# Performance work log

Hardware: AMD Instinct MI355X
Metric: run time of the kernel (lower is better)

The kernel has to match this reference:

```python
import jax, jax.numpy as jnp
import numpy as np


def setup_inputs() -> dict:
    key = jax.random.key(0)
    ks = jax.random.split(key, 6)
    B, T, E, H, K = 4, 2048, 1024, 16, 3
    x = jax.random.normal(ks[0], (B, T, E), dtype=jnp.float32)
    mem_k = jax.random.normal(ks[1], (B, T, K, E), dtype=jnp.float32)
    mem_v = jax.random.normal(ks[2], (B, T, K, E), dtype=jnp.float32)
    W_attn = jax.random.normal(ks[3], (E, 3 * E), dtype=jnp.float32) * 0.02
    W_proj = jax.random.normal(ks[4], (E, E), dtype=jnp.float32) * 0.02
    gate_bias = jax.random.normal(ks[5], (H, 1, 1), dtype=jnp.float32)
    return {"x": x, "mem_k": mem_k, "mem_v": mem_v, "W_attn": W_attn,
            "W_proj": W_proj, "gate_bias": gate_bias}


def reference(x, mem_k, mem_v, W_attn, W_proj, gate_bias):
    B, T, E = x.shape
    H = gate_bias.shape[0]
    D = E // H
    K = mem_k.shape[2]
    # qkv projection (no bias)
    qkv = x @ W_attn                                   # [B,T,3E]
    q, k, v = jnp.split(qkv, 3, axis=-1)
    q = q.reshape(B, T, H, D).transpose(0, 2, 1, 3)    # [B,H,T,D]
    k = k.reshape(B, T, H, D).transpose(0, 2, 1, 3)
    v = v.reshape(B, T, H, D).transpose(0, 2, 1, 3)
    # causal SDPA (torch default scale = 1/sqrt(head_dim))
    scores = jnp.einsum('bhqd,bhkd->bhqk', q, k) / jnp.sqrt(jnp.asarray(D, q.dtype))
    causal = jnp.tril(jnp.ones((T, T), dtype=bool))
    scores = jnp.where(causal, scores, jnp.finfo(scores.dtype).min)
    attn = jax.nn.softmax(scores, axis=-1)
    y = jnp.einsum('bhqk,bhkd->bhqd', attn, v)         # [B,H,T,D]
    # top-k retrieved memory attention (k small, here 3)
    mk = mem_k.reshape(B, T, K, H, D).transpose(0, 3, 1, 2, 4)  # [B,H,T,K,D]
    mv = mem_v.reshape(B, T, K, H, D).transpose(0, 3, 1, 2, 4)
    # faithful to source: scale = n_embd / n_head**(-0.5) = E*sqrt(H)
    mem_scale = jnp.asarray(E, q.dtype) * jnp.sqrt(jnp.asarray(H, q.dtype))
    mem_qk = jnp.einsum('bhtd,bhtkd->bhtk', q, mk) * mem_scale
    mem_qk = jax.nn.softmax(mem_qk, axis=-1)
    mem_qkv = jnp.einsum('bhtk,bhtkd->bhtd', mem_qk, mv)  # [B,H,T,D]
    # gated fusion, gate_bias broadcasts [H,1,1] over [B,H,T,D]
    combined = mem_qkv * gate_bias + y * (1.0 - gate_bias)
    combined = combined.transpose(0, 2, 1, 3).reshape(B, T, E)
    out = combined @ W_proj
    return out
```

## Files before the change

### kernel.cpp

```cpp
#include <hip/hip_runtime.h>
#include <math.h>

#define Bsz 4
#define Tseq 2048
#define Ed 1024
#define Hh 16
#define E3 (3*Ed)
#define MROWS (Bsz*Tseq)

typedef short short8 __attribute__((ext_vector_type(8)));
typedef _Float16 half8 __attribute__((ext_vector_type(8)));
typedef float floatx4 __attribute__((ext_vector_type(4)));

__device__ __forceinline__ unsigned short f2bf(float f) {
  unsigned int u = __builtin_bit_cast(unsigned int, f);
  u += 0x7fffu + ((u >> 16) & 1u);
  return (unsigned short)(u >> 16);
}
__device__ __forceinline__ float bf2f(unsigned short u) {
  return __builtin_bit_cast(float, ((unsigned int)u) << 16);
}
__device__ __forceinline__ unsigned short f2h(float f) {
  _Float16 h = (_Float16)f;
  return __builtin_bit_cast(unsigned short, h);
}
__device__ __forceinline__ float h2f(unsigned short u) {
  return (float)__builtin_bit_cast(_Float16, u);
}
__device__ __forceinline__ int swz(int row, int col) {
  return row * 64 + ((((col >> 3) ^ (row & 7)) << 3) | (col & 7));
}

__global__ __launch_bounds__(256)
void cast_split_k(const float* __restrict__ s, unsigned short* __restrict__ bb,
                  unsigned short* __restrict__ hh, unsigned short* __restrict__ ll,
                  int n4) {
  int i = blockIdx.x * 256 + threadIdx.x;
  if (i >= n4) return;
  float4 v = ((const float4*)s)[i];
  float vv[4] = {v.x, v.y, v.z, v.w};
  unsigned short ob[4], oh[4], ol[4];
  #pragma unroll
  for (int j = 0; j < 4; ++j) {
    ob[j] = f2bf(vv[j]);
    unsigned short h = f2h(vv[j]);
    oh[j] = h;
    ol[j] = f2h(vv[j] - h2f(h));
  }
  ((uint2*)bb)[i] = *(uint2*)ob;
  ((uint2*)hh)[i] = *(uint2*)oh;
  ((uint2*)ll)[i] = *(uint2*)ol;
}

__global__ __launch_bounds__(256)
void transpose_cast(const float* __restrict__ src, int ld, int c0,
                    unsigned short* __restrict__ dst, int Krows) {
  __shared__ float t[64][65];
  const int kb = blockIdx.y * 64, nb = blockIdx.x * 64;
  const int tid = threadIdx.x;
  #pragma unroll
  for (int i = 0; i < 4; ++i) {
    int u = tid + i * 256;
    int r = u >> 4, c4 = u & 15;
    float4 v = *(const float4*)(src + (size_t)(kb + r) * ld + c0 + nb + c4 * 4);
    t[r][c4*4+0] = v.x; t[r][c4*4+1] = v.y; t[r][c4*4+2] = v.z; t[r][c4*4+3] = v.w;
  }
  __syncthreads();
  #pragma unroll
  for (int i = 0; i < 2; ++i) {
    int u = tid + i * 256;
    int rn = u >> 3, g = u & 7;
    unsigned short o[8];
    #pragma unroll
    for (int j = 0; j < 8; ++j) o[j] = f2bf(t[g*8+j][rn]);
    *(uint4*)(dst + (size_t)(nb + rn) * Krows + kb + g * 8) = *(uint4*)o;
  }
}

__global__ __launch_bounds__(256)
void transpose_split(const float* __restrict__ src, int ld, int c0,
                     unsigned short* __restrict__ dh, unsigned short* __restrict__ dl,
                     int Krows) {
  __shared__ float t[64][65];
  const int kb = blockIdx.y * 64, nb = blockIdx.x * 64;
  const int tid = threadIdx.x;
  #pragma unroll
  for (int i = 0; i < 4; ++i) {
    int u = tid + i * 256;
    int r = u >> 4, c4 = u & 15;
    float4 v = *(const float4*)(src + (size_t)(kb + r) * ld + c0 + nb + c4 * 4);
    t[r][c4*4+0] = v.x; t[r][c4*4+1] = v.y; t[r][c4*4+2] = v.z; t[r][c4*4+3] = v.w;
  }
  __syncthreads();
  #pragma unroll
  for (int i = 0; i < 2; ++i) {
    int u = tid + i * 256;
    int rn = u >> 3, g = u & 7;
    unsigned short oh[8], ol[8];
    #pragma unroll
    for (int j = 0; j < 8; ++j) {
      float f = t[g*8+j][rn];
      unsigned short h = f2h(f);
      oh[j] = h;
      ol[j] = f2h(f - h2f(h));
    }
    size_t off = (size_t)(nb + rn) * Krows + kb + g * 8;
    *(uint4*)(dh + off) = *(uint4*)oh;
    *(uint4*)(dl + off) = *(uint4*)ol;
  }
}

template<int N, int KD, bool OBF>
__global__ __launch_bounds__(256)
void gemm_bf16(const unsigned short* __restrict__ A,
               const unsigned short* __restrict__ Bt,
               void* __restrict__ C) {
  __shared__ __align__(16) unsigned short As[128][72];
  __shared__ __align__(16) unsigned short Bs[128][72];
  const int tid = threadIdx.x;
  const int w = tid >> 6, L = tid & 63, Ln = L & 15, Lq = L >> 4;
  const int wm = w & 1, wn = w >> 1;
  const int m0 = blockIdx.y * 128, n0 = blockIdx.x * 128;

  floatx4 acc[4][4];
  #pragma unroll
  for (int mt = 0; mt < 4; ++mt)
    #pragma unroll
    for (int nt = 0; nt < 4; ++nt) acc[mt][nt] = (floatx4)0.f;

  for (int kt = 0; kt < KD; kt += 64) {
    #pragma unroll
    for (int i = 0; i < 4; ++i) {
      int u = tid + i * 256;
      int row = u >> 3, g = u & 7;
      *(uint4*)&As[row][g*8] = *(const uint4*)(A + (size_t)(m0 + row) * KD + kt + g * 8);
      *(uint4*)&Bs[row][g*8] = *(const uint4*)(Bt + (size_t)(n0 + row) * KD + kt + g * 8);
    }
    __syncthreads();
    #pragma unroll
    for (int kc = 0; kc < 2; ++kc) {
      short8 af[4], bfr[4];
      #pragma unroll
      for (int mt = 0; mt < 4; ++mt)
        af[mt] = *(const short8*)&As[wm*64 + mt*16 + Ln][kc*32 + Lq*8];
      #pragma unroll
      for (int nt = 0; nt < 4; ++nt)
        bfr[nt] = *(const short8*)&Bs[wn*64 + nt*16 + Ln][kc*32 + Lq*8];
      #pragma unroll
      for (int mt = 0; mt < 4; ++mt)
        #pragma unroll
        for (int nt = 0; nt < 4; ++nt)
          acc[mt][nt] = __builtin_amdgcn_mfma_f32_16x16x32_bf16(af[mt], bfr[nt], acc[mt][nt], 0, 0, 0);
    }
    __syncthreads();
  }
  #pragma unroll
  for (int mt = 0; mt < 4; ++mt)
    #pragma unroll
    for (int nt = 0; nt < 4; ++nt)
      #pragma unroll
      for (int r = 0; r < 4; ++r) {
        size_t row = m0 + wm*64 + mt*16 + Lq*4 + r;
        int col = n0 + wn*64 + nt*16 + Ln;
        if (OBF) ((unsigned short*)C)[row * N + col] = f2bf(acc[mt][nt][r]);
        else     ((float*)C)[row * N + col] = acc[mt][nt][r];
      }
}

template<int N, int KD>
__global__ __launch_bounds__(256)
void gemm_f16x3(const unsigned short* __restrict__ Ah,
                const unsigned short* __restrict__ Al,
                const unsigned short* __restrict__ Bh,
                const unsigned short* __restrict__ Bl,
                float* __restrict__ C) {
  __shared__ __align__(16) unsigned short As[2][128][40];
  __shared__ __align__(16) unsigned short Bs[2][128][40];
  const int tid = threadIdx.x;
  const int w = tid >> 6, L = tid & 63, Ln = L & 15, Lq = L >> 4;
  const int wm = w & 1, wn = w >> 1;
  const int m0 = blockIdx.y * 128, n0 = blockIdx.x * 128;

  floatx4 acc[4][4];
  #pragma unroll
  for (int mt = 0; mt < 4; ++mt)
    #pragma unroll
    for (int nt = 0; nt < 4; ++nt) acc[mt][nt] = (floatx4)0.f;

  for (int kt = 0; kt < KD; kt += 32) {
    #pragma unroll
    for (int i = 0; i < 2; ++i) {
      int u = tid + i * 256;
      int row = u >> 2, g = u & 3;
      size_t offA = (size_t)(m0 + row) * KD + kt + g * 8;
      size_t offB = (size_t)(n0 + row) * KD + kt + g * 8;
      *(uint4*)&As[0][row][g*8] = *(const uint4*)(Ah + offA);
      *(uint4*)&As[1][row][g*8] = *(const uint4*)(Al + offA);
      *(uint4*)&Bs[0][row][g*8] = *(const uint4*)(Bh + offB);
      *(uint4*)&Bs[1][row][g*8] = *(const uint4*)(Bl + offB);
    }
    __syncthreads();
    half8 afh[4], afl[4], bfh[4], bfl[4];
    #pragma unroll
    for (int mt = 0; mt < 4; ++mt) {
      afh[mt] = *(const half8*)&As[0][wm*64 + mt*16 + Ln][Lq*8];
      afl[mt] = *(const half8*)&As[1][wm*64 + mt*16 + Ln][Lq*8];
    }
    #pragma unroll
    for (int nt = 0; nt < 4; ++nt) {
      bfh[nt] = *(const half8*)&Bs[0][wn*64 + nt*16 + Ln][Lq*8];
      bfl[nt] = *(const half8*)&Bs[1][wn*64 + nt*16 + Ln][Lq*8];
    }
    #pragma unroll
    for (int mt = 0; mt < 4; ++mt)
      #pragma unroll
      for (int nt = 0; nt < 4; ++nt) {
        acc[mt][nt] = __builtin_amdgcn_mfma_f32_16x16x32_f16(afh[mt], bfh[nt], acc[mt][nt], 0, 0, 0);
        acc[mt][nt] = __builtin_amdgcn_mfma_f32_16x16x32_f16(afh[mt], bfl[nt], acc[mt][nt], 0, 0, 0);
        acc[mt][nt] = __builtin_amdgcn_mfma_f32_16x16x32_f16(afl[mt], bfh[nt], acc[mt][nt], 0, 0, 0);
      }
    __syncthreads();
  }
  #pragma unroll
  for (int mt = 0; mt < 4; ++mt)
    #pragma unroll
    for (int nt = 0; nt < 4; ++nt)
      #pragma unroll
      for (int r = 0; r < 4; ++r) {
        size_t row = m0 + wm*64 + mt*16 + Lq*4 + r;
        int col = n0 + wn*64 + nt*16 + Ln;
        C[row * N + col] = acc[mt][nt][r];
      }
}

__global__ __launch_bounds__(256)
void flash_mfma(const float* __restrict__ qf, const unsigned short* __restrict__ kv,
                unsigned short* __restrict__ y) {
  __shared__ __align__(16) unsigned short Ks[2][64 * 64];
  __shared__ __align__(16) unsigned short Vt[2][64 * 64];
  __shared__ __align__(16) unsigned short Ps[4][32 * 64];
  const int ib = blockIdx.x;
  const int bh = blockIdx.y;
  const int b = bh >> 4, h = bh & 15;
  const int tid = threadIdx.x;
  const int w = tid >> 6, L = tid & 63;
  const int Ln = L & 15, Lq = L >> 4;
  const size_t base = (size_t)b * Tseq;
  const int hof = h * 64;

  for (int t = 0; t < 2; ++t) {
    const int qt = t ? ib : 15 - ib;
    const int q0 = qt * 128;
    const int nkt = 2 * qt + 2;

    short8 qfr[2][2];
    #pragma unroll
    for (int mt = 0; mt < 2; ++mt) {
      const float* qp = qf + (base + q0 + w*32 + mt*16 + Ln) * Ed + hof;
      #pragma unroll
      for (int kc = 0; kc < 2; ++kc) {
        float v[8];
        *(float4*)&v[0] = *(const float4*)(qp + kc*32 + Lq*8);
        *(float4*)&v[4] = *(const float4*)(qp + kc*32 + Lq*8 + 4);
        short8 tt;
        #pragma unroll
        for (int j = 0; j < 8; ++j) tt[j] = (short)f2bf(v[j]);
        qfr[mt][kc] = tt;
      }
    }

    float m_i[2][4], l_i[2][4];
    floatx4 O[2][4];
    #pragma unroll
    for (int mt = 0; mt < 2; ++mt) {
      #pragma unroll
      for (int r = 0; r < 4; ++r) { m_i[mt][r] = -3.0e38f; l_i[mt][r] = 0.f; }
      #pragma unroll
      for (int nt = 0; nt < 4; ++nt) O[mt][nt] = (floatx4)0.f;
    }

    #pragma unroll
    for (int i = 0; i < 2; ++i) {
      int u = tid + i * 256;
      int c = u >> 3, g = u & 7;
      const unsigned short* kvp = kv + (base + c) * 2048 + hof + g * 8;
      uint4 k4 = *(const uint4*)kvp;
      *(uint4*)&Ks[0][c*64 + ((g ^ (c & 7)) << 3)] = k4;
      unsigned short vv[8];
      *(uint4*)vv = *(const uint4*)(kvp + 1024);
      #pragma unroll
      for (int j = 0; j < 8; ++j) Vt[0][swz(g*8 + j, c)] = vv[j];
    }
    __syncthreads();

    int cur = 0;
    for (int kt = 0; kt < nkt; ++kt) {
      uint4 kreg[2], vreg[2];
      const bool pre = (kt + 1 < nkt);
      if (pre) {
        #pragma unroll
        for (int i = 0; i < 2; ++i) {
          int u = tid + i * 256;
          int c = u >> 3, g = u & 7;
          const unsigned short* kvp = kv + (base + (kt+1)*64 + c) * 2048 + hof + g * 8;
          kreg[i] = *(const uint4*)kvp;
          vreg[i] = *(const uint4*)(kvp + 1024);
        }
      }

      short8 kb[4][2];
      #pragma unroll
      for (int nt = 0; nt < 4; ++nt) {
        int krow = nt*16 + Ln;
        #pragma unroll
        for (int kc = 0; kc < 2; ++kc)
          kb[nt][kc] = *(const short8*)&Ks[cur][krow*64 + ((((kc*4 + Lq) ^ (krow & 7)) << 3))];
      }
      floatx4 S[2][4];
      #pragma unroll
      for (int mt = 0; mt < 2; ++mt)
        #pragma unroll
        for (int nt = 0; nt < 4; ++nt) {
          floatx4 a = (floatx4)0.f;
          a = __builtin_amdgcn_mfma_f32_16x16x32_bf16(qfr[mt][0], kb[nt][0], a, 0, 0, 0);
          a = __builtin_amdgcn_mfma_f32_16x16x32_bf16(qfr[mt][1], kb[nt][1], a, 0, 0, 0);
          S[mt][nt] = a;
        }
      #pragma unroll
      for (int mt = 0; mt < 2; ++mt)
        #pragma unroll
        for (int nt = 0; nt < 4; ++nt)
          #pragma unroll
          for (int r = 0; r < 4; ++r) S[mt][nt][r] *= 0.125f;
      if (kt >= 2*qt) {
        #pragma unroll
        for (int mt = 0; mt < 2; ++mt) {
          int rowg = q0 + w*32 + mt*16 + Lq*4;
          #pragma unroll
          for (int nt = 0; nt < 4; ++nt) {
            int colg = kt*64 + nt*16 + Ln;
            #pragma unroll
            for (int r = 0; r < 4; ++r)
              if (colg > rowg + r) S[mt][nt][r] = -3.0e38f;
          }
        }
      }

      #pragma unroll
      for (int mt = 0; mt < 2; ++mt) {
        #pragma unroll
        for (int r = 0; r < 4; ++r) {
          float mx = fmaxf(fmaxf(S[mt][0][r], S[mt][1][r]),
                           fmaxf(S[mt][2][r], S[mt][3][r]));
          mx = fmaxf(mx, __shfl_xor(mx, 1));
          mx = fmaxf(mx, __shfl_xor(mx, 2));
          mx = fmaxf(mx, __shfl_xor(mx, 4));
          mx = fmaxf(mx, __shfl_xor(mx, 8));
          float mnew = fmaxf(m_i[mt][r], mx);
          float alpha = __expf(m_i[mt][r] - mnew);
          m_i[mt][r] = mnew;
          float rs = 0.f;
          #pragma unroll
          for (int nt = 0; nt < 4; ++nt) {
            float p = __expf(S[mt][nt][r] - mnew);
            S[mt][nt][r] = p;
            rs += p;
          }
          rs += __shfl_xor(rs, 1);
          rs += __shfl_xor(rs, 2);
          rs += __shfl_xor(rs, 4);
          rs += __shfl_xor(rs, 8);
          l_i[mt][r] = l_i[mt][r] * alpha + rs;
          #pragma unroll
          for (int nt = 0; nt < 4; ++nt) O[mt][nt][r] *= alpha;
          int prow = mt*16 + Lq*4 + r;
          #pragma unroll
          for (int nt = 0; nt < 4; ++nt)
            Ps[w][swz(prow, nt*16 + Ln)] = f2bf(S[mt][nt][r]);
        }
      }

      short8 vb[4][2], pf[2][2];
      #pragma unroll
      for (int nt = 0; nt < 4; ++nt) {
        int vrow = nt*16 + Ln;
        #pragma unroll
        for (int kc = 0; kc < 2; ++kc)
          vb[nt][kc] = *(const short8*)&Vt[cur][vrow*64 + ((((kc*4 + Lq) ^ (vrow & 7)) << 3))];
      }
      #pragma unroll
      for (int mt = 0; mt < 2; ++mt) {
        int prow = mt*16 + Ln;
        #pragma unroll
        for (int kc = 0; kc < 2; ++kc)
          pf[mt][kc] = *(const short8*)&Ps[w][prow*64 + ((((kc*4 + Lq) ^ (prow & 7)) << 3))];
      }
      #pragma unroll
      for (int mt = 0; mt < 2; ++mt)
        #pragma unroll
        for (int nt = 0; nt < 4; ++nt) {
          O[mt][nt] = __builtin_amdgcn_mfma_f32_16x16x32_bf16(pf[mt][0], vb[nt][0], O[mt][nt], 0, 0, 0);
          O[mt][nt] = __builtin_amdgcn_mfma_f32_16x16x32_bf16(pf[mt][1], vb[nt][1], O[mt][nt], 0, 0, 0);
        }

      if (pre) {
        #pragma unroll
        for (int i = 0; i < 2; ++i) {
          int u = tid + i * 256;
          int c = u >> 3, g = u & 7;
          *(uint4*)&Ks[cur^1][c*64 + ((g ^ (c & 7)) << 3)] = kreg[i];
          unsigned short vv[8];
          *(uint4*)vv = vreg[i];
          #pragma unroll
          for (int j = 0; j < 8; ++j) Vt[cur^1][swz(g*8 + j, c)] = vv[j];
        }
      }
      __syncthreads();
      cur ^= 1;
    }

    #pragma unroll
    for (int mt = 0; mt < 2; ++mt) {
      #pragma unroll
      for (int r = 0; r < 4; ++r) {
        float inv = 1.f / l_i[mt][r];
        size_t rb = (base + q0 + w*32 + mt*16 + Lq*4 + r) * Ed + hof;
        #pragma unroll
        for (int nt = 0; nt < 4; ++nt)
          y[rb + nt*16 + Ln] = f2bf(O[mt][nt][r] * inv);
      }
    }
  }
}

__global__ __launch_bounds__(256)
void mem_gate(const float* __restrict__ qf, const float* __restrict__ mem_k,
              const float* __restrict__ mem_v, const float* __restrict__ gate,
              unsigned short* __restrict__ y) {
  const int tid = threadIdx.x;
  const int lane = tid & 63;
  const int g = (blockIdx.x << 2) | (tid >> 6);
  const int h = g & 15;
  const int bt = g >> 4;
  const float q = qf[(size_t)bt * Ed + h*64 + lane];
  const size_t mb = ((size_t)bt * 3) * Ed + h*64 + lane;

  float s[3];
  #pragma unroll
  for (int k = 0; k < 3; ++k) {
    float p = q * mem_k[mb + (size_t)k * Ed];
    p += __shfl_xor(p, 1);  p += __shfl_xor(p, 2);  p += __shfl_xor(p, 4);
    p += __shfl_xor(p, 8);  p += __shfl_xor(p, 16); p += __shfl_xor(p, 32);
    s[k] = p * 4096.0f;
  }
  float mx = fmaxf(s[0], fmaxf(s[1], s[2]));
  float w0 = __expf(s[0] - mx), w1 = __expf(s[1] - mx), w2 = __expf(s[2] - mx);
  float inv = 1.f / (w0 + w1 + w2);
  float ov = (w0 * mem_v[mb] + w1 * mem_v[mb + Ed] + w2 * mem_v[mb + 2*Ed]) * inv;
  float gb = gate[h];
  unsigned short* yp = y + (size_t)bt * Ed + h*64 + lane;
  float yv = bf2f(*yp);
  *yp = f2bf(ov * gb + yv * (1.f - gb));
}

extern "C" void kernel_launch(void* const* d_in, const int* in_sizes, int n_in,
                              void* d_out, int out_size, void* d_ws, size_t ws_size,
                              hipStream_t stream) {
  const float* x      = (const float*)d_in[0];
  const float* mem_k  = (const float*)d_in[1];
  const float* mem_v  = (const float*)d_in[2];
  const float* W_attn = (const float*)d_in[3];
  const float* W_proj = (const float*)d_in[4];
  const float* gate   = (const float*)d_in[5];
  float* out = (float*)d_out;

  float* qf32          = (float*)d_ws;
  unsigned short* kvb  = (unsigned short*)(qf32 + (size_t)MROWS*Ed);
  unsigned short* ybf  = kvb + (size_t)MROWS*2048;
  unsigned short* xb   = ybf + (size_t)MROWS*Ed;
  unsigned short* wkv  = xb  + (size_t)MROWS*Ed;
  unsigned short* wp   = wkv + (size_t)2048*Ed;
  unsigned short* xh  = (unsigned short*)d_out;
  unsigned short* xl  = xh + (size_t)MROWS*Ed;
  unsigned short* wqh = kvb;
  unsigned short* wql = wqh + (size_t)Ed*Ed;

  cast_split_k<<<(MROWS*Ed/4 + 255)/256, 256, 0, stream>>>(x, xb, xh, xl, MROWS*Ed/4);
  transpose_split<<<dim3(Ed/64, Ed/64), 256, 0, stream>>>(W_attn, E3, 0, wqh, wql, Ed);
  transpose_cast<<<dim3(2048/64, Ed/64), 256, 0, stream>>>(W_attn, E3, Ed, wkv, Ed);
  transpose_cast<<<dim3(Ed/64, Ed/64), 256, 0, stream>>>(W_proj, Ed, 0, wp, Ed);
  gemm_f16x3<Ed, Ed>
      <<<dim3(Ed/128, MROWS/128), 256, 0, stream>>>(xh, xl, wqh, wql, qf32);
  gemm_bf16<2048, Ed, true>
      <<<dim3(2048/128, MROWS/128), 256, 0, stream>>>(xb, wkv, kvb);
  flash_mfma<<<dim3(8, Bsz*Hh), 256, 0, stream>>>(qf32, kvb, ybf);
  mem_gate<<<(MROWS*Hh)/4, 256, 0, stream>>>(qf32, mem_k, mem_v, gate, ybf);
  gemm_bf16<Ed, Ed, false>
      <<<dim3(Ed/128, MROWS/128), 256, 0, stream>>>(ybf, wp, out);
}
```

Measured before the change: 608.5 us.

## Split flash attention query tile across eight waves of sixteen rows

The flash attention kernel now launches 512 threads per block, and each of eight waves owns 16 query rows instead of four waves owning 32 rows. Per-wave register state (O, S, m, l) halves and the K/V tile load is spread over twice as many threads. The intent is more latency hiding through higher wave count per CU. The cost is that every wave reloads the same K/V fragments from LDS for half the MFMA work, so LDS traffic per FLOP roughly doubles.

Measured after the change: 528.4 us. -13.2%, faster.

```diff
diff --git a/kernel.cpp b/kernel.cpp
--- a/kernel.cpp
+++ b/kernel.cpp
@@ -233,12 +233,12 @@
       }
 }
 
-__global__ __launch_bounds__(256)
+__global__ __launch_bounds__(512, 4)
 void flash_mfma(const float* __restrict__ qf, const unsigned short* __restrict__ kv,
                 unsigned short* __restrict__ y) {
   __shared__ __align__(16) unsigned short Ks[2][64 * 64];
   __shared__ __align__(16) unsigned short Vt[2][64 * 64];
-  __shared__ __align__(16) unsigned short Ps[4][32 * 64];
+  __shared__ __align__(16) unsigned short Ps[8][16 * 64];
   const int ib = blockIdx.x;
   const int bh = blockIdx.y;
   const int b = bh >> 4, h = bh & 15;
@@ -253,10 +253,9 @@
     const int q0 = qt * 128;
     const int nkt = 2 * qt + 2;
 
-    short8 qfr[2][2];
-    #pragma unroll
-    for (int mt = 0; mt < 2; ++mt) {
-      const float* qp = qf + (base + q0 + w*32 + mt*16 + Ln) * Ed + hof;
+    short8 qfr[2];
+    {
+      const float* qp = qf + (base + q0 + w*16 + Ln) * Ed + hof;
       #pragma unroll
       for (int kc = 0; kc < 2; ++kc) {
         float v[8];
@@ -265,24 +264,19 @@
         short8 tt;
         #pragma unroll
         for (int j = 0; j < 8; ++j) tt[j] = (short)f2bf(v[j]);
-        qfr[mt][kc] = tt;
-      }
-    }
-
-    float m_i[2][4], l_i[2][4];
-    floatx4 O[2][4];
-    #pragma unroll
-    for (int mt = 0; mt < 2; ++mt) {
-      #pragma unroll
-      for (int r = 0; r < 4; ++r) { m_i[mt][r] = -3.0e38f; l_i[mt][r] = 0.f; }
-      #pragma unroll
-      for (int nt = 0; nt < 4; ++nt) O[mt][nt] = (floatx4)0.f;
-    }
-
-    #pragma unroll
-    for (int i = 0; i < 2; ++i) {
-      int u = tid + i * 256;
-      int c = u >> 3, g = u & 7;
+        qfr[kc] = tt;
+      }
+    }
+
+    float m_i[4], l_i[4];
+    floatx4 O[4];
+    #pragma unroll
+    for (int r = 0; r < 4; ++r) { m_i[r] = -3.0e38f; l_i[r] = 0.f; }
+    #pragma unroll
+    for (int nt = 0; nt < 4; ++nt) O[nt] = (floatx4)0.f;
+
+    {
+      int c = tid >> 3, g = tid & 7;
       const unsigned short* kvp = kv + (base + c) * 2048 + hof + g * 8;
       uint4 k4 = *(const uint4*)kvp;
       *(uint4*)&Ks[0][c*64 + ((g ^ (c & 7)) << 3)] = k4;
@@ -295,17 +289,13 @@
 
     int cur = 0;
     for (int kt = 0; kt < nkt; ++kt) {
-      uint4 kreg[2], vreg[2];
+      uint4 kreg, vreg;
       const bool pre = (kt + 1 < nkt);
+      const int c = tid >> 3, g = tid & 7;
       if (pre) {
-        #pragma unroll
-        for (int i = 0; i < 2; ++i) {
-          int u = tid + i * 256;
-          int c = u >> 3, g = u & 7;
-          const unsigned short* kvp = kv + (base + (kt+1)*64 + c) * 2048 + hof + g * 8;
-          kreg[i] = *(const uint4*)kvp;
-          vreg[i] = *(const uint4*)(kvp + 1024);
-        }
+        const unsigned short* kvp = kv + (base + (kt+1)*64 + c) * 2048 + hof + g * 8;
+        kreg = *(const uint4*)kvp;
+        vreg = *(const uint4*)(kvp + 1024);
       }
 
       short8 kb[4][2];
@@ -316,71 +306,60 @@
         for (int kc = 0; kc < 2; ++kc)
           kb[nt][kc] = *(const short8*)&Ks[cur][krow*64 + ((((kc*4 + Lq) ^ (krow & 7)) << 3))];
       }
-      floatx4 S[2][4];
-      #pragma unroll
-      for (int mt = 0; mt < 2; ++mt)
+      floatx4 S[4];
+      #pragma unroll
+      for (int nt = 0; nt < 4; ++nt) {
+        floatx4 a = (floatx4)0.f;
+        a = __builtin_amdgcn_mfma_f32_16x16x32_bf16(qfr[0], kb[nt][0], a, 0, 0, 0);
+        a = __builtin_amdgcn_mfma_f32_16x16x32_bf16(qfr[1], kb[nt][1], a, 0, 0, 0);
+        S[nt] = a;
+      }
+      #pragma unroll
+      for (int nt = 0; nt < 4; ++nt)
+        #pragma unroll
+        for (int r = 0; r < 4; ++r) S[nt][r] *= 0.125f;
+      if (kt >= 2*qt) {
+        int rowg = q0 + w*16 + Lq*4;
         #pragma unroll
         for (int nt = 0; nt < 4; ++nt) {
-          floatx4 a = (floatx4)0.f;
-          a = __builtin_amdgcn_mfma_f32_16x16x32_bf16(qfr[mt][0], kb[nt][0], a, 0, 0, 0);
-          a = __builtin_amdgcn_mfma_f32_16x16x32_bf16(qfr[mt][1], kb[nt][1], a, 0, 0, 0);
-          S[mt][nt] = a;
+          int colg = kt*64 + nt*16 + Ln;
+          #pragma unroll
+          for (int r = 0; r < 4; ++r)
+            if (colg > rowg + r) S[nt][r] = -3.0e38f;
         }
-      #pragma unroll
-      for (int mt = 0; mt < 2; ++mt)
+      }
+
+      #pragma unroll
+      for (int r = 0; r < 4; ++r) {
+        float mx = fmaxf(fmaxf(S[0][r], S[1][r]), fmaxf(S[2][r], S[3][r]));
+        mx = fmaxf(mx, __shfl_xor(mx, 1));
+        mx = fmaxf(mx, __shfl_xor(mx, 2));
+        mx = fmaxf(mx, __shfl_xor(mx, 4));
+        mx = fmaxf(mx, __shfl_xor(mx, 8));
+        float mnew = fmaxf(m_i[r], mx);
+        float alpha = __expf(m_i[r] - mnew);
+        m_i[r] = mnew;
+        float rs = 0.f;
+        #pragma unroll
+        for (int nt = 0; nt < 4; ++nt) {
+          float p = __expf(S[nt][r] - mnew);
+          S[nt][r] = p;
+          rs += p;
+        }
+        rs += __shfl_xor(rs, 1);
+        rs += __shfl_xor(rs, 2);
+        rs += __shfl_xor(rs, 4);
+        rs += __shfl_xor(rs, 8);
+        l_i[r] = l_i[r] * alpha + rs;
+        #pragma unroll
+        for (int nt = 0; nt < 4; ++nt) O[nt][r] *= alpha;
+        int prow = Lq*4 + r;
         #pragma unroll
         for (int nt = 0; nt < 4; ++nt)
-          #pragma unroll
-          for (int r = 0; r < 4; ++r) S[mt][nt][r] *= 0.125f;
-      if (kt >= 2*qt) {
-        #pragma unroll
-        for (int mt = 0; mt < 2; ++mt) {
-          int rowg = q0 + w*32 + mt*16 + Lq*4;
-          #pragma unroll
-          for (int nt = 0; nt < 4; ++nt) {
-            int colg = kt*64 + nt*16 + Ln;
-            #pragma unroll
-            for (int r = 0; r < 4; ++r)
-              if (colg > rowg + r) S[mt][nt][r] = -3.0e38f;
-          }
-        }
-      }
-
-      #pragma unroll
-      for (int mt = 0; mt < 2; ++mt) {
-        #pragma unroll
-        for (int r = 0; r < 4; ++r) {
-          float mx = fmaxf(fmaxf(S[mt][0][r], S[mt][1][r]),
-                           fmaxf(S[mt][2][r], S[mt][3][r]));
-          mx = fmaxf(mx, __shfl_xor(mx, 1));
-          mx = fmaxf(mx, __shfl_xor(mx, 2));
-          mx = fmaxf(mx, __shfl_xor(mx, 4));
-          mx = fmaxf(mx, __shfl_xor(mx, 8));
-          float mnew = fmaxf(m_i[mt][r], mx);
-          float alpha = __expf(m_i[mt][r] - mnew);
-          m_i[mt][r] = mnew;
-          float rs = 0.f;
-          #pragma unroll
-          for (int nt = 0; nt < 4; ++nt) {
-            float p = __expf(S[mt][nt][r] - mnew);
-            S[mt][nt][r] = p;
-            rs += p;
-          }
-          rs += __shfl_xor(rs, 1);
-          rs += __shfl_xor(rs, 2);
-          rs += __shfl_xor(rs, 4);
-          rs += __shfl_xor(rs, 8);
-          l_i[mt][r] = l_i[mt][r] * alpha + rs;
-          #pragma unroll
-          for (int nt = 0; nt < 4; ++nt) O[mt][nt][r] *= alpha;
-          int prow = mt*16 + Lq*4 + r;
-          #pragma unroll
-          for (int nt = 0; nt < 4; ++nt)
-            Ps[w][swz(prow, nt*16 + Ln)] = f2bf(S[mt][nt][r]);
-        }
-      }
-
-      short8 vb[4][2], pf[2][2];
+          Ps[w][swz(prow, nt*16 + Ln)] = f2bf(S[nt][r]);
+      }
+
+      short8 vb[4][2], pf[2];
       #pragma unroll
       for (int nt = 0; nt < 4; ++nt) {
         int vrow = nt*16 + Ln;
@@ -388,47 +367,36 @@
         for (int kc = 0; kc < 2; ++kc)
           vb[nt][kc] = *(const short8*)&Vt[cur][vrow*64 + ((((kc*4 + Lq) ^ (vrow & 7)) << 3))];
       }
-      #pragma unroll
-      for (int mt = 0; mt < 2; ++mt) {
-        int prow = mt*16 + Ln;
+      {
+        int prow = Ln;
         #pragma unroll
         for (int kc = 0; kc < 2; ++kc)
-          pf[mt][kc] = *(const short8*)&Ps[w][prow*64 + ((((kc*4 + Lq) ^ (prow & 7)) << 3))];
-      }
-      #pragma unroll
-      for (int mt = 0; mt < 2; ++mt)
-        #pragma unroll
-        for (int nt = 0; nt < 4; ++nt) {
-          O[mt][nt] = __builtin_amdgcn_mfma_f32_16x16x32_bf16(pf[mt][0], vb[nt][0], O[mt][nt], 0, 0, 0);
-          O[mt][nt] = __builtin_amdgcn_mfma_f32_16x16x32_bf16(pf[mt][1], vb[nt][1], O[mt][nt], 0, 0, 0);
-        }
+          pf[kc] = *(const short8*)&Ps[w][prow*64 + ((((kc*4 + Lq) ^ (prow & 7)) << 3))];
+      }
+      #pragma unroll
+      for (int nt = 0; nt < 4; ++nt) {
+        O[nt] = __builtin_amdgcn_mfma_f32_16x16x32_bf16(pf[0], vb[nt][0], O[nt], 0, 0, 0);
+        O[nt] = __builtin_amdgcn_mfma_f32_16x16x32_bf16(pf[1], vb[nt][1], O[nt], 0, 0, 0);
+      }
 
       if (pre) {
-        #pragma unroll
-        for (int i = 0; i < 2; ++i) {
-          int u = tid + i * 256;
-          int c = u >> 3, g = u & 7;
-          *(uint4*)&Ks[cur^1][c*64 + ((g ^ (c & 7)) << 3)] = kreg[i];
-          unsigned short vv[8];
-          *(uint4*)vv = vreg[i];
-          #pragma unroll
-          for (int j = 0; j < 8; ++j) Vt[cur^1][swz(g*8 + j, c)] = vv[j];
-        }
+        *(uint4*)&Ks[cur^1][c*64 + ((g ^ (c & 7)) << 3)] = kreg;
+        unsigned short vv[8];
+        *(uint4*)vv = vreg;
+        #pragma unroll
+        for (int j = 0; j < 8; ++j) Vt[cur^1][swz(g*8 + j, c)] = vv[j];
       }
       __syncthreads();
       cur ^= 1;
     }
 
     #pragma unroll
-    for (int mt = 0; mt < 2; ++mt) {
-      #pragma unroll
-      for (int r = 0; r < 4; ++r) {
-        float inv = 1.f / l_i[mt][r];
-        size_t rb = (base + q0 + w*32 + mt*16 + Lq*4 + r) * Ed + hof;
-        #pragma unroll
-        for (int nt = 0; nt < 4; ++nt)
-          y[rb + nt*16 + Ln] = f2bf(O[mt][nt][r] * inv);
-      }
+    for (int r = 0; r < 4; ++r) {
+      float inv = 1.f / l_i[r];
+      size_t rb = (base + q0 + w*16 + Lq*4 + r) * Ed + hof;
+      #pragma unroll
+      for (int nt = 0; nt < 4; ++nt)
+        y[rb + nt*16 + Ln] = f2bf(O[nt][r] * inv);
     }
   }
 }
@@ -493,7 +461,7 @@
       <<<dim3(Ed/128, MROWS/128), 256, 0, stream>>>(xh, xl, wqh, wql, qf32);
   gemm_bf16<2048, Ed, true>
       <<<dim3(2048/128, MROWS/128), 256, 0, stream>>>(xb, wkv, kvb);
-  flash_mfma<<<dim3(8, Bsz*Hh), 256, 0, stream>>>(qf32, kvb, ybf);
+  flash_mfma<<<dim3(8, Bsz*Hh), 512, 0, stream>>>(qf32, kvb, ybf);
   mem_gate<<<(MROWS*Hh)/4, 256, 0, stream>>>(qf32, mem_k, mem_v, gate, ybf);
   gemm_bf16<Ed, Ed, false>
       <<<dim3(Ed/128, MROWS/128), 256, 0, stream>>>(ybf, wp, out);
```
